# Performance work log

Hardware: AMD Instinct MI355X
Metric: run time of the kernel (lower is better)

## Reference

```python
import jax, jax.numpy as jnp
import numpy as np

NUM_KNOTS = 64
HEAD_DIM = 4
SCALE = 0.5  # 1/sqrt(4)


def setup_inputs() -> dict:
    key = jax.random.key(0)
    ks = jax.random.split(key, 6)
    B, L, D = 4, 128, 256
    s = 1.0 / np.sqrt(D)
    return {
        "x": jax.random.normal(ks[0], (B, L, D), dtype=jnp.float32),
        "Wq": jax.random.normal(ks[1], (D, D), dtype=jnp.float32) * s,
        "Wk": jax.random.normal(ks[2], (D, D), dtype=jnp.float32) * s,
        "Wv": jax.random.normal(ks[3], (D, D), dtype=jnp.float32) * s,
        "Wo": jax.random.normal(ks[4], (D, D), dtype=jnp.float32) * s,
        "bo": jnp.zeros((D,), dtype=jnp.float32),
    }


def reference(x, Wq, Wk, Wv, Wo, bo):
    # x: [B, L, D], D = NUM_KNOTS * HEAD_DIM = 256
    B, L, D = x.shape
    N = L * NUM_KNOTS  # flattened 'knot' sequence length
    # nn.Linear applies x @ W.T
    q = (x @ Wq.T).reshape(B, N, HEAD_DIM)
    k = (x @ Wk.T).reshape(B, N, HEAD_DIM)
    v = (x @ Wv.T).reshape(B, N, HEAD_DIM)
    # full attention over the length-N knot sequence (head_dim = 4)
    logits = jnp.einsum("bnd,bmd->bnm", q, k) * SCALE  # [B, N, N]
    attn = jax.nn.softmax(logits, axis=-1)
    out = jnp.einsum("bnm,bmd->bnd", attn, v).reshape(B, L, D)
    return out @ Wo.T + bo
```

## Files before the change

kernel.cpp:

```cpp
#include <hip/hip_runtime.h>

#define NQ 8192
#define BLROWS 512
#define DIM 256

#define QSCALE 0.7213475204444817f

typedef float v2f __attribute__((ext_vector_type(2)));

__device__ __forceinline__ float ex2(float x) {
#if __has_builtin(__builtin_amdgcn_exp2f)
    return __builtin_amdgcn_exp2f(x);
#else
    return exp2f(x);
#endif
}

__device__ __forceinline__ void proj4_body(
    const float* __restrict__ A, const float* __restrict__ W,
    const float* __restrict__ bias, float* __restrict__ C,
    float scale, int rb)
{
    const int j = threadIdx.x;
    float acc[4] = {0.f, 0.f, 0.f, 0.f};
    const float4* __restrict__ W4 = reinterpret_cast<const float4*>(W + j * DIM);
    const float*  __restrict__ A0 = A + rb * DIM;

    #pragma unroll 4
    for (int d4 = 0; d4 < DIM / 4; ++d4) {
        const float4 w = W4[d4];
        #pragma unroll
        for (int r = 0; r < 4; ++r) {
            const float4 a = reinterpret_cast<const float4*>(A0 + r * DIM)[d4];
            acc[r] = fmaf(a.x, w.x, acc[r]);
            acc[r] = fmaf(a.y, w.y, acc[r]);
            acc[r] = fmaf(a.z, w.z, acc[r]);
            acc[r] = fmaf(a.w, w.w, acc[r]);
        }
    }
    const float b = bias ? bias[j] : 0.f;
    #pragma unroll
    for (int r = 0; r < 4; ++r)
        C[(rb + r) * DIM + j] = fmaf(acc[r], scale, b);
}

__global__ __launch_bounds__(256) void qkv_proj(
    const float* __restrict__ x,
    const float* __restrict__ Wq, const float* __restrict__ Wk,
    const float* __restrict__ Wv,
    float* __restrict__ Qb, float* __restrict__ Kb, float* __restrict__ Vb)
{
    const int m = blockIdx.y;
    const float* W = (m == 0) ? Wq : (m == 1) ? Wk : Wv;
    float* C       = (m == 0) ? Qb : (m == 1) ? Kb : Vb;
    const float sc = (m == 0) ? QSCALE : 1.0f;
    proj4_body(x, W, nullptr, C, sc, blockIdx.x * 4);
}

__global__ __launch_bounds__(256) void proj4_kernel(
    const float* __restrict__ A, const float* __restrict__ W,
    const float* __restrict__ bias, float* __restrict__ C, float scale)
{
    proj4_body(A, W, bias, C, scale, blockIdx.x * 4);
}

__global__ __launch_bounds__(1024, 4) void attn_partial(
    const float* __restrict__ Q, const float* __restrict__ K,
    const float* __restrict__ V, float* __restrict__ P)
{
    const int lane = threadIdx.x & 63;
    const int w    = threadIdx.x >> 6;
    const int qt   = blockIdx.x;
    const int ks   = blockIdx.y;
    const int b    = blockIdx.z;

    const float4* __restrict__ Qp = reinterpret_cast<const float4*>(Q) + b * NQ + qt * 512;
    const float4* __restrict__ Kp = reinterpret_cast<const float4*>(K) + b * NQ + ks * 1024 + w * 64;
    const float4* __restrict__ Vp = reinterpret_cast<const float4*>(V) + b * NQ + ks * 1024 + w * 64;

    v2f qx[4], qy[4], qz[4], qw[4];
    #pragma unroll
    for (int p = 0; p < 4; ++p) {
        const float4 t0 = Qp[(2 * p)     * 64 + lane];
        const float4 t1 = Qp[(2 * p + 1) * 64 + lane];
        qx[p] = v2f{t0.x, t1.x};
        qy[p] = v2f{t0.y, t1.y};
        qz[p] = v2f{t0.z, t1.z};
        qw[p] = v2f{t0.w, t1.w};
    }
    v2f a0[4], a1[4], a2[4], a3[4], ls[4];
    #pragma unroll
    for (int p = 0; p < 4; ++p) {
        a0[p] = v2f{0.f, 0.f}; a1[p] = v2f{0.f, 0.f};
        a2[p] = v2f{0.f, 0.f}; a3[p] = v2f{0.f, 0.f};
        ls[p] = v2f{0.f, 0.f};
    }

    #pragma unroll 2
    for (int j = 0; j < 64; ++j) {
        const float4 k4 = Kp[j];
        const float4 v4 = Vp[j];
        const v2f kx = v2f{k4.x, k4.x}, ky = v2f{k4.y, k4.y};
        const v2f kz = v2f{k4.z, k4.z}, kw = v2f{k4.w, k4.w};
        const v2f vx = v2f{v4.x, v4.x}, vy = v2f{v4.y, v4.y};
        const v2f vz = v2f{v4.z, v4.z}, vw = v2f{v4.w, v4.w};
        #pragma unroll
        for (int p = 0; p < 4; ++p) {
            v2f s = qx[p] * kx;
            s = __builtin_elementwise_fma(qy[p], ky, s);
            s = __builtin_elementwise_fma(qz[p], kz, s);
            s = __builtin_elementwise_fma(qw[p], kw, s);
            const v2f e = v2f{ex2(s[0]), ex2(s[1])};
            ls[p] += e;
            a0[p] = __builtin_elementwise_fma(e, vx, a0[p]);
            a1[p] = __builtin_elementwise_fma(e, vy, a1[p]);
            a2[p] = __builtin_elementwise_fma(e, vz, a2[p]);
            a3[p] = __builtin_elementwise_fma(e, vw, a3[p]);
        }
    }

    __shared__ float red[4][512][5];
    #pragma unroll 1
    for (int ph = 0; ph < 4; ++ph) {
        if ((w >> 2) == ph) {
            #pragma unroll
            for (int p = 0; p < 4; ++p) {
                #pragma unroll
                for (int e = 0; e < 2; ++e) {
                    float* pr = &red[w & 3][(2 * p + e) * 64 + lane][0];
                    if (ph == 0) {
                        pr[0] = ls[p][e]; pr[1] = a0[p][e]; pr[2] = a1[p][e];
                        pr[3] = a2[p][e]; pr[4] = a3[p][e];
                    } else {
                        pr[0] += ls[p][e]; pr[1] += a0[p][e]; pr[2] += a1[p][e];
                        pr[3] += a2[p][e]; pr[4] += a3[p][e];
                    }
                }
            }
        }
        __syncthreads();
    }

    float* __restrict__ Pb = P + (size_t)((b * 8 + ks) * 5) * NQ + qt * 512;
    const int qq = threadIdx.x;
    if (qq < 512) {
        #pragma unroll
        for (int c = 0; c < 5; ++c) {
            const float sred = red[0][qq][c] + red[1][qq][c] + red[2][qq][c] + red[3][qq][c];
            Pb[c * NQ + qq] = sred;
        }
    }
}

__global__ __launch_bounds__(256) void attn_merge(
    const float* __restrict__ P, float* __restrict__ AO)
{
    const int idx = blockIdx.x * 256 + threadIdx.x;
    const int b = idx >> 13;
    const int n = idx & (NQ - 1);
    float l = 0.f, x0 = 0.f, x1 = 0.f, x2 = 0.f, x3 = 0.f;
    #pragma unroll
    for (int s = 0; s < 8; ++s) {
        const float* Pb = P + (size_t)((b * 8 + s) * 5) * NQ + n;
        l  += Pb[0];
        x0 += Pb[NQ];
        x1 += Pb[2 * NQ];
        x2 += Pb[3 * NQ];
        x3 += Pb[4 * NQ];
    }
    const float inv = 1.0f / l;
    reinterpret_cast<float4*>(AO)[idx] = make_float4(x0 * inv, x1 * inv, x2 * inv, x3 * inv);
}

extern "C" void kernel_launch(void* const* d_in, const int* in_sizes, int n_in,
                              void* d_out, int out_size, void* d_ws, size_t ws_size,
                              hipStream_t stream) {
    const float* x  = (const float*)d_in[0];
    const float* Wq = (const float*)d_in[1];
    const float* Wk = (const float*)d_in[2];
    const float* Wv = (const float*)d_in[3];
    const float* Wo = (const float*)d_in[4];
    const float* bo = (const float*)d_in[5];
    float* out = (float*)d_out;

    float* Qb = (float*)d_ws;
    float* Kb = Qb + BLROWS * DIM;
    float* Vb = Kb + BLROWS * DIM;
    float* AO = Vb + BLROWS * DIM;
    float* P  = AO + BLROWS * DIM;

    qkv_proj<<<dim3(128, 3), 256, 0, stream>>>(x, Wq, Wk, Wv, Qb, Kb, Vb);
    attn_partial<<<dim3(16, 8, 4), 1024, 0, stream>>>(Qb, Kb, Vb, P);
    attn_merge<<<128, 256, 0, stream>>>(P, AO);
    proj4_kernel<<<128, 256, 0, stream>>>(AO, Wo, bo, out, 1.0f);
}
```

Measured before the change: 102.0 us.

## Shrink attention blocks to 256 threads with 256 queries and longer key loops

Result: faster. 91.94 us (-9.8%).

```diff
diff --git a/kernel.cpp b/kernel.cpp
--- a/kernel.cpp
+++ b/kernel.cpp
@@ -64,23 +64,23 @@
     proj4_body(A, W, bias, C, scale, blockIdx.x * 4);
 }
 
-__global__ __launch_bounds__(1024, 4) void attn_partial(
+__global__ __launch_bounds__(256) void attn_partial(
     const float* __restrict__ Q, const float* __restrict__ K,
     const float* __restrict__ V, float* __restrict__ P)
 {
     const int lane = threadIdx.x & 63;
-    const int w    = threadIdx.x >> 6;
+    const int w    = __builtin_amdgcn_readfirstlane(threadIdx.x >> 6);
     const int qt   = blockIdx.x;
     const int ks   = blockIdx.y;
     const int b    = blockIdx.z;
 
-    const float4* __restrict__ Qp = reinterpret_cast<const float4*>(Q) + b * NQ + qt * 512;
-    const float4* __restrict__ Kp = reinterpret_cast<const float4*>(K) + b * NQ + ks * 1024 + w * 64;
-    const float4* __restrict__ Vp = reinterpret_cast<const float4*>(V) + b * NQ + ks * 1024 + w * 64;
+    const float4* __restrict__ Qp = reinterpret_cast<const float4*>(Q) + b * NQ + qt * 256;
+    const float4* __restrict__ Kp = reinterpret_cast<const float4*>(K) + b * NQ + ks * 1024 + w * 256;
+    const float4* __restrict__ Vp = reinterpret_cast<const float4*>(V) + b * NQ + ks * 1024 + w * 256;
 
-    v2f qx[4], qy[4], qz[4], qw[4];
+    v2f qx[2], qy[2], qz[2], qw[2];
     #pragma unroll
-    for (int p = 0; p < 4; ++p) {
+    for (int p = 0; p < 2; ++p) {
         const float4 t0 = Qp[(2 * p)     * 64 + lane];
         const float4 t1 = Qp[(2 * p + 1) * 64 + lane];
         qx[p] = v2f{t0.x, t1.x};
@@ -88,67 +88,51 @@
         qz[p] = v2f{t0.z, t1.z};
         qw[p] = v2f{t0.w, t1.w};
     }
-    v2f a0[4], a1[4], a2[4], a3[4], ls[4];
+    v2f a0[2], a1[2], a2[2], a3[2], ls[2];
     #pragma unroll
-    for (int p = 0; p < 4; ++p) {
+    for (int p = 0; p < 2; ++p) {
         a0[p] = v2f{0.f, 0.f}; a1[p] = v2f{0.f, 0.f};
         a2[p] = v2f{0.f, 0.f}; a3[p] = v2f{0.f, 0.f};
         ls[p] = v2f{0.f, 0.f};
     }
 
-    #pragma unroll 2
-    for (int j = 0; j < 64; ++j) {
+    #pragma unroll 8
+    for (int j = 0; j < 256; ++j) {
         const float4 k4 = Kp[j];
         const float4 v4 = Vp[j];
-        const v2f kx = v2f{k4.x, k4.x}, ky = v2f{k4.y, k4.y};
-        const v2f kz = v2f{k4.z, k4.z}, kw = v2f{k4.w, k4.w};
-        const v2f vx = v2f{v4.x, v4.x}, vy = v2f{v4.y, v4.y};
-        const v2f vz = v2f{v4.z, v4.z}, vw = v2f{v4.w, v4.w};
         #pragma unroll
-        for (int p = 0; p < 4; ++p) {
-            v2f s = qx[p] * kx;
-            s = __builtin_elementwise_fma(qy[p], ky, s);
-            s = __builtin_elementwise_fma(qz[p], kz, s);
-            s = __builtin_elementwise_fma(qw[p], kw, s);
+        for (int p = 0; p < 2; ++p) {
+            v2f s = qx[p] * k4.x;
+            s = __builtin_elementwise_fma(qy[p], v2f{k4.y, k4.y}, s);
+            s = __builtin_elementwise_fma(qz[p], v2f{k4.z, k4.z}, s);
+            s = __builtin_elementwise_fma(qw[p], v2f{k4.w, k4.w}, s);
             const v2f e = v2f{ex2(s[0]), ex2(s[1])};
             ls[p] += e;
-            a0[p] = __builtin_elementwise_fma(e, vx, a0[p]);
-            a1[p] = __builtin_elementwise_fma(e, vy, a1[p]);
-            a2[p] = __builtin_elementwise_fma(e, vz, a2[p]);
-            a3[p] = __builtin_elementwise_fma(e, vw, a3[p]);
+            a0[p] = __builtin_elementwise_fma(e, v2f{v4.x, v4.x}, a0[p]);
+            a1[p] = __builtin_elementwise_fma(e, v2f{v4.y, v4.y}, a1[p]);
+            a2[p] = __builtin_elementwise_fma(e, v2f{v4.z, v4.z}, a2[p]);
+            a3[p] = __builtin_elementwise_fma(e, v2f{v4.w, v4.w}, a3[p]);
         }
     }
 
-    __shared__ float red[4][512][5];
-    #pragma unroll 1
-    for (int ph = 0; ph < 4; ++ph) {
-        if ((w >> 2) == ph) {
-            #pragma unroll
-            for (int p = 0; p < 4; ++p) {
-                #pragma unroll
-                for (int e = 0; e < 2; ++e) {
-                    float* pr = &red[w & 3][(2 * p + e) * 64 + lane][0];
-                    if (ph == 0) {
-                        pr[0] = ls[p][e]; pr[1] = a0[p][e]; pr[2] = a1[p][e];
-                        pr[3] = a2[p][e]; pr[4] = a3[p][e];
-                    } else {
-                        pr[0] += ls[p][e]; pr[1] += a0[p][e]; pr[2] += a1[p][e];
-                        pr[3] += a2[p][e]; pr[4] += a3[p][e];
-                    }
-                }
-            }
+    __shared__ float red[4][256][5];
+    #pragma unroll
+    for (int p = 0; p < 2; ++p) {
+        #pragma unroll
+        for (int e = 0; e < 2; ++e) {
+            float* pr = &red[w][(2 * p + e) * 64 + lane][0];
+            pr[0] = ls[p][e]; pr[1] = a0[p][e]; pr[2] = a1[p][e];
+            pr[3] = a2[p][e]; pr[4] = a3[p][e];
         }
-        __syncthreads();
     }
+    __syncthreads();
 
-    float* __restrict__ Pb = P + (size_t)((b * 8 + ks) * 5) * NQ + qt * 512;
+    float* __restrict__ Pb = P + (size_t)((b * 8 + ks) * 5) * NQ + qt * 256;
     const int qq = threadIdx.x;
-    if (qq < 512) {
-        #pragma unroll
-        for (int c = 0; c < 5; ++c) {
-            const float sred = red[0][qq][c] + red[1][qq][c] + red[2][qq][c] + red[3][qq][c];
-            Pb[c * NQ + qq] = sred;
-        }
+    #pragma unroll
+    for (int c = 0; c < 5; ++c) {
+        const float sred = red[0][qq][c] + red[1][qq][c] + red[2][qq][c] + red[3][qq][c];
+        Pb[c * NQ + qq] = sred;
     }
 }
 
@@ -190,7 +174,7 @@
     float* P  = AO + BLROWS * DIM;
 
     qkv_proj<<<dim3(128, 3), 256, 0, stream>>>(x, Wq, Wk, Wv, Qb, Kb, Vb);
-    attn_partial<<<dim3(16, 8, 4), 1024, 0, stream>>>(Qb, Kb, Vb, P);
+    attn_partial<<<dim3(32, 8, 4), 256, 0, stream>>>(Qb, Kb, Vb, P);
     attn_merge<<<128, 256, 0, stream>>>(P, AO);
     proj4_kernel<<<128, 256, 0, stream>>>(AO, Wo, bo, out, 1.0f);
 }
```
